# Kernel optimization log

Measured on AMD Instinct MI355X. Metric: run time of the kernel, lower is better.

## Reference

```python
import jax, jax.numpy as jnp
import numpy as np

C, L, M, DEPTH = 32, 4, 128, 7
DIM = (L ** (DEPTH + 1) - 1) // (L - 1)  # 21845 nodes, complete 4-ary tree, BFS order


def _level_starts(dim, fanout):
    # start offset of each BFS level of a complete `fanout`-ary tree
    starts = [0]
    n = 1
    while starts[-1] + n < dim:
        starts.append(starts[-1] + n)
        n *= fanout
    starts.append(dim)
    return starts  # level d occupies [starts[d], starts[d+1])


def setup_inputs() -> dict:
    key = jax.random.key(0)
    ks = jax.random.split(key, 5)
    return {
        "labels": jax.random.randint(ks[0], (DIM,), 0, M, dtype=jnp.int32),
        "A": jax.random.normal(ks[1], (C, C, L), jnp.float32),
        "B": jax.random.normal(ks[2], (C, M), jnp.float32),
        "Pi": jax.random.normal(ks[3], (C, L), jnp.float32),
        "SP": jax.random.normal(ks[4], (L,), jnp.float32),
    }


def _htmm_log_likelihood(labels, A, B, Pi, SP):
    dim = labels.shape[0]
    c, m = B.shape
    fan = A.shape[2]
    starts = _level_starts(dim, fan)
    D = len(starts) - 2  # deepest level index (leaves)

    # softmax reparameterization (dims as in torch source)
    smA = jax.nn.softmax(A, axis=0)   # (C,C,L)
    smB = jax.nn.softmax(B, axis=1)   # (C,M)
    smPi = jax.nn.softmax(Pi, axis=0)  # (C,L)
    smSP = jax.nn.softmax(SP, axis=0)  # (L,)

    n_leaves = starts[D + 1] - starts[D]
    leaf_pos = jnp.arange(n_leaves) % fan          # child position of each leaf
    leaf_labels = labels[starts[D]:]

    # ---- upward pass ----
    beta_leaf = smPi[:, leaf_pos].T * smB[:, leaf_labels].T  # (n_leaves,C)
    beta_leaf = beta_leaf / beta_leaf.sum(1, keepdims=True)
    beta = jnp.zeros((dim, c), A.dtype).at[starts[D]:].set(beta_leaf)
    t_beta = jnp.zeros((dim, c), A.dtype)
    A_SP = smA * smSP[None, None, :]  # (C,C,L): SP[pos] * A[:,:,pos]

    for d in range(D - 1, -1, -1):
        n_p = starts[d + 1] - starts[d]
        beta_ch = beta[starts[d + 1]:starts[d + 2]].reshape(n_p, fan, c)  # (P,L,C)
        # t_beta_u[i] = sum_l SP[l] * sum_j A[i,j,l] * beta_child_l[j]
        tb = jnp.einsum('ijl,plj->pi', A_SP, beta_ch)  # (P,C)
        bl = tb * smB[:, labels[starts[d]:starts[d + 1]]].T
        bl = bl / bl.sum(1, keepdims=True)
        t_beta = t_beta.at[starts[d]:starts[d + 1]].set(tb)
        beta = beta.at[starts[d]:starts[d + 1]].set(bl)

    # ---- downward pass ----
    eps = jnp.zeros((dim, c), A.dtype).at[0].set(beta[0])
    t_eps = jnp.zeros((dim, c, c, fan), A.dtype)
    for d in range(D):
        n_p = starts[d + 1] - starts[d]
        beta_ch = beta[starts[d + 1]:starts[d + 2]].reshape(n_p, fan, c)  # (P,L,C)
        eps_pa = eps[starts[d]:starts[d + 1]]    # (P,C)
        tb_pa = t_beta[starts[d]:starts[d + 1]]  # (P,C)
        # t_eps_u[j,i,l] = beta[ch_l,i] * SP[l]*A[j,i,l] * eps_u[j] / t_beta_u[j]
        te = (beta_ch.transpose(0, 2, 1)[:, None, :, :]   # (P,1,C_i,L)
              * A_SP[None]                                  # (1,C_j,C_i,L)
              * (eps_pa / tb_pa)[:, :, None, None])         # (P,C_j,1,1)
        t_eps = t_eps.at[starts[d]:starts[d + 1]].set(te)
        eps_ch = te.sum(1).transpose(0, 2, 1).reshape(-1, c)  # sum_j -> (P,L,C) -> (P*L,C)
        eps = eps.at[starts[d + 1]:starts[d + 2]].set(eps_ch)

    # ---- log-likelihood ----
    ll = (t_eps * jnp.log(smA)[None]).sum()
    ll = ll + (eps * jnp.log(smB)[:, labels].T).sum()
    ll = ll + (eps[starts[D]:] * jnp.log(smPi)[:, leaf_pos].T).sum()
    ll = ll + (t_eps * jnp.log(smSP)[None, None, None, :]).sum()
    return ll


def reference(labels, A, B, Pi, SP):
    return _htmm_log_likelihood(labels, A, B, Pi, SP)
```

## Files before the change

### kernel.cpp

```cpp
#include <hip/hip_runtime.h>


static constexpr int OFF_B4   = 0;
static constexpr int OFF_PART = 8192;
static constexpr int IC1      = 8704;
static constexpr int IROOT1   = 9216;
static constexpr int IREL     = 9248;
static constexpr int IC2      = 9760;
static constexpr int IROOT2   = 10272;

__device__ __forceinline__ float rsum32(float v) {
#pragma unroll
  for (int k = 1; k <= 16; k <<= 1) v += __shfl_xor(v, k);
  return v;
}
__device__ __forceinline__ void rsum32x2(float& a, float& b) {
#pragma unroll
  for (int k = 1; k <= 16; k <<= 1) { a += __shfl_xor(a, k); b += __shfl_xor(b, k); }
}
__device__ __forceinline__ void rsum32x4(float& a, float& b, float& c, float& d) {
#pragma unroll
  for (int k = 1; k <= 16; k <<= 1) {
    a += __shfl_xor(a, k); b += __shfl_xor(b, k);
    c += __shfl_xor(c, k); d += __shfl_xor(d, k);
  }
}
__device__ __forceinline__ float4 exp4f(float4 v) {
  return make_float4(__expf(v.x), __expf(v.y), __expf(v.z), __expf(v.w));
}

__device__ __forceinline__ float dot128(const float* Wr, const float* X) {
  float t0 = 0.f, t1 = 0.f, t2 = 0.f, t3 = 0.f;
#pragma unroll
  for (int j = 0; j < 32; ++j) {
    const float4 x = *(const float4*)(X + j * 4);
    t0 = fmaf(Wr[4 * j + 0], x.x, t0);
    t1 = fmaf(Wr[4 * j + 1], x.y, t1);
    t2 = fmaf(Wr[4 * j + 2], x.z, t2);
    t3 = fmaf(Wr[4 * j + 3], x.w, t3);
  }
  return (t0 + t1) + (t2 + t3);
}
__device__ __forceinline__ void dot128x2(const float* Wr, const float* X0,
                                         const float* X1, float& o0, float& o1) {
  float a0 = 0.f, a1 = 0.f, a2 = 0.f, a3 = 0.f;
  float b0 = 0.f, b1 = 0.f, b2 = 0.f, b3 = 0.f;
#pragma unroll
  for (int j = 0; j < 32; ++j) {
    const float4 x = *(const float4*)(X0 + j * 4);
    const float4 y = *(const float4*)(X1 + j * 4);
    a0 = fmaf(Wr[4 * j + 0], x.x, a0); b0 = fmaf(Wr[4 * j + 0], y.x, b0);
    a1 = fmaf(Wr[4 * j + 1], x.y, a1); b1 = fmaf(Wr[4 * j + 1], y.y, b1);
    a2 = fmaf(Wr[4 * j + 2], x.z, a2); b2 = fmaf(Wr[4 * j + 2], y.z, b2);
    a3 = fmaf(Wr[4 * j + 3], x.w, a3); b3 = fmaf(Wr[4 * j + 3], y.w, b3);
  }
  o0 = (a0 + a1) + (a2 + a3);
  o1 = (b0 + b1) + (b2 + b3);
}

__device__ __forceinline__ void wu128(const float* Wr, const float* ALG,
                                      const float* rb, int lane,
                                      float w[4], float u[4]) {
  w[0] = w[1] = w[2] = w[3] = 0.f;
  u[0] = u[1] = u[2] = u[3] = 0.f;
#pragma unroll
  for (int ii = 0; ii < 32; ii += 4) {
    const float4 rv = *(const float4*)(rb + ii);
#pragma unroll
    for (int di = 0; di < 4; ++di) {
      const int i = ii + di;
      const float rr = (di == 0) ? rv.x : (di == 1) ? rv.y : (di == 2) ? rv.z : rv.w;
      const float4 av = *(const float4*)(ALG + i * 128 + lane * 4);
      w[0] = fmaf(Wr[i * 4 + 0], rr, w[0]); u[0] = fmaf(av.x, rr, u[0]);
      w[1] = fmaf(Wr[i * 4 + 1], rr, w[1]); u[1] = fmaf(av.y, rr, u[1]);
      w[2] = fmaf(Wr[i * 4 + 2], rr, w[2]); u[2] = fmaf(av.z, rr, u[2]);
      w[3] = fmaf(Wr[i * 4 + 3], rr, w[3]); u[3] = fmaf(av.w, rr, u[3]);
    }
  }
}
__device__ __forceinline__ void wu128x2(const float* Wr, const float* ALG,
                                        const float* rb0, const float* rb1, int lane,
                                        float w0[4], float u0[4],
                                        float w1[4], float u1[4]) {
#pragma unroll
  for (int l = 0; l < 4; ++l) { w0[l] = u0[l] = w1[l] = u1[l] = 0.f; }
#pragma unroll
  for (int ii = 0; ii < 32; ii += 4) {
    const float4 r0 = *(const float4*)(rb0 + ii);
    const float4 r1 = *(const float4*)(rb1 + ii);
#pragma unroll
    for (int di = 0; di < 4; ++di) {
      const int i = ii + di;
      const float q0 = (di == 0) ? r0.x : (di == 1) ? r0.y : (di == 2) ? r0.z : r0.w;
      const float q1 = (di == 0) ? r1.x : (di == 1) ? r1.y : (di == 2) ? r1.z : r1.w;
      const float4 av = *(const float4*)(ALG + i * 128 + lane * 4);
      w0[0] = fmaf(Wr[i * 4 + 0], q0, w0[0]); w1[0] = fmaf(Wr[i * 4 + 0], q1, w1[0]);
      u0[0] = fmaf(av.x, q0, u0[0]);          u1[0] = fmaf(av.x, q1, u1[0]);
      w0[1] = fmaf(Wr[i * 4 + 1], q0, w0[1]); w1[1] = fmaf(Wr[i * 4 + 1], q1, w1[1]);
      u0[1] = fmaf(av.y, q0, u0[1]);          u1[1] = fmaf(av.y, q1, u1[1]);
      w0[2] = fmaf(Wr[i * 4 + 2], q0, w0[2]); w1[2] = fmaf(Wr[i * 4 + 2], q1, w1[2]);
      u0[2] = fmaf(av.z, q0, u0[2]);          u1[2] = fmaf(av.z, q1, u1[2]);
      w0[3] = fmaf(Wr[i * 4 + 3], q0, w0[3]); w1[3] = fmaf(Wr[i * 4 + 3], q1, w1[3]);
      u0[3] = fmaf(av.w, q0, u0[3]);          u1[3] = fmaf(av.w, q1, u1[3]);
    }
  }
}
__device__ __forceinline__ void wonly128(const float* Wr, const float* rb,
                                         float w[4]) {
  w[0] = w[1] = w[2] = w[3] = 0.f;
#pragma unroll
  for (int ii = 0; ii < 32; ii += 4) {
    const float4 rv = *(const float4*)(rb + ii);
#pragma unroll
    for (int di = 0; di < 4; ++di) {
      const int i = ii + di;
      const float rr = (di == 0) ? rv.x : (di == 1) ? rv.y : (di == 2) ? rv.z : rv.w;
      w[0] = fmaf(Wr[i * 4 + 0], rr, w[0]);
      w[1] = fmaf(Wr[i * 4 + 1], rr, w[1]);
      w[2] = fmaf(Wr[i * 4 + 2], rr, w[2]);
      w[3] = fmaf(Wr[i * 4 + 3], rr, w[3]);
    }
  }
}

__global__ __launch_bounds__(256, 1) void k_up(const int* __restrict__ labels,
                                               const float* __restrict__ A,
                                               const float* __restrict__ B,
                                               const float* __restrict__ Pi,
                                               const float* __restrict__ SP,
                                               float* __restrict__ ws) {
  __shared__ __align__(16) float scr[4224];
  __shared__ __align__(16) float regB[4224];
  __shared__ __align__(16) float sPt[132];
  __shared__ int labs[425];
  const int t = threadIdx.x, lane = t & 31, grp = t >> 5;
  const int s = blockIdx.x;
  const float4* A4 = (const float4*)A;
  const float4* B4 = (const float4*)B;

  const float sv0 = SP[0], sv1 = SP[1], sv2 = SP[2], sv3 = SP[3];
  const float sp0 = __expf(sv0), sp1 = __expf(sv1), sp2 = __expf(sv2), sp3 = __expf(sv3);
  const float spsum = sp0 + sp1 + sp2 + sp3;
  const float spinv = 1.f / spsum;
  float4 c4 = make_float4(0.f, 0.f, 0.f, 0.f);
  for (int i = 0; i < 32; ++i) {
    const float4 e = exp4f(A4[i * 32 + lane]);
    c4.x += e.x; c4.y += e.y; c4.z += e.z; c4.w += e.w;
  }
  const float4 inv4 = make_float4(sp0 * spinv / c4.x, sp1 * spinv / c4.y,
                                  sp2 * spinv / c4.z, sp3 * spinv / c4.w);
#pragma unroll
  for (int k = 0; k < 4; ++k) {
    const int i = grp * 4 + k;
    const float4 e = exp4f(A4[i * 32 + lane]);
    *(float4*)(scr + i * 132 + 4 * lane) =
        make_float4(e.x * inv4.x, e.y * inv4.y, e.z * inv4.z, e.w * inv4.w);
  }
#pragma unroll
  for (int rI = 0; rI < 4; ++rI) {
    const int i = grp + rI * 8;
    const float4 e = exp4f(B4[i * 32 + lane]);
    const float sinv = 1.f / rsum32(e.x + e.y + e.z + e.w);
    regB[(4 * lane + 0) * 33 + i] = e.x * sinv;
    regB[(4 * lane + 1) * 33 + i] = e.y * sinv;
    regB[(4 * lane + 2) * 33 + i] = e.z * sinv;
    regB[(4 * lane + 3) * 33 + i] = e.w * sinv;
  }
  if (grp < 4) {
    const float e = __expf(Pi[lane * 4 + grp]);
    sPt[grp * 33 + lane] = e / rsum32(e);
  }
  if (t < 84) {
    int g, d;
    if (t < 4) { g = 341 + 4 * s + t; d = 341 + t; }
    else if (t < 20) { g = 1365 + 16 * s + (t - 4); d = 345 + (t - 4); }
    else { g = 5461 + 64 * s + (t - 20); d = 361 + (t - 20); }
    labs[d] = labels[g];
  }
  if (t == 84) labs[85 + (s & 255)] = labels[85 + s];
  __syncthreads();
  float Wr[128];
#pragma unroll
  for (int j = 0; j < 32; ++j) {
    const float4 v = *(const float4*)(scr + lane * 132 + j * 4);
    Wr[4 * j] = v.x; Wr[4 * j + 1] = v.y; Wr[4 * j + 2] = v.z; Wr[4 * j + 3] = v.w;
  }
  __syncthreads();

#pragma unroll
  for (int h = 0; h < 2; ++h) {
    const int q0 = grp + 32 * h, q1 = q0 + 8, q2 = q0 + 16, q3 = q0 + 24;
    float v0 = sPt[(q0 & 3) * 33 + lane] * regB[labs[361 + q0] * 33 + lane];
    float v1 = sPt[(q1 & 3) * 33 + lane] * regB[labs[361 + q1] * 33 + lane];
    float v2 = sPt[(q2 & 3) * 33 + lane] * regB[labs[361 + q2] * 33 + lane];
    float v3 = sPt[(q3 & 3) * 33 + lane] * regB[labs[361 + q3] * 33 + lane];
    float s0 = v0, s1 = v1, s2 = v2, s3 = v3;
    rsum32x4(s0, s1, s2, s3);
    scr[(q0 >> 2) * 128 + lane * 4 + (q0 & 3)] = v0 / s0;
    scr[(q1 >> 2) * 128 + lane * 4 + (q1 & 3)] = v1 / s1;
    scr[(q2 >> 2) * 128 + lane * 4 + (q2 & 3)] = v2 / s2;
    scr[(q3 >> 2) * 128 + lane * 4 + (q3 & 3)] = v3 / s3;
  }
  __syncthreads();
  {
    const int p0 = grp, p1 = grp + 8;
    float tb0, tb1;
    dot128x2(Wr, scr + p0 * 128, scr + p1 * 128, tb0, tb1);
    float bl0 = tb0 * regB[labs[345 + p0] * 33 + lane];
    float bl1 = tb1 * regB[labs[345 + p1] * 33 + lane];
    float s0 = bl0, s1 = bl1;
    rsum32x2(s0, s1);
    bl0 /= s0; bl1 /= s1;
    scr[2048 + (p0 >> 2) * 128 + lane * 4 + (p0 & 3)] = bl0;
    scr[2048 + (p1 >> 2) * 128 + lane * 4 + (p1 & 3)] = bl1;
  }
  __syncthreads();
  if (grp < 4) {
    const float tb = dot128(Wr, scr + 2048 + grp * 128);
    float bl = tb * regB[labs[341 + grp] * 33 + lane];
    bl /= rsum32(bl);
    scr[2560 + lane * 4 + grp] = bl;
  }
  __syncthreads();
  if (grp == 0) {
    const float tb = dot128(Wr, scr + 2560);
    float bl = tb * regB[labs[85 + (s & 255)] * 33 + lane];
    bl /= rsum32(bl);
    ws[OFF_B4 + s * 32 + lane] = bl;
  }
}

__global__ __launch_bounds__(256, 1) void k_down(const int* __restrict__ labels,
                                                 const float* __restrict__ A,
                                                 const float* __restrict__ B,
                                                 const float* __restrict__ Pi,
                                                 const float* __restrict__ SP,
                                                 float* __restrict__ ws,
                                                 float* __restrict__ out) {
  __shared__ __align__(16) float scr[4224];
  __shared__ __align__(16) float regB[4224];
  __shared__ __align__(16) float sPt[132];
  __shared__ __align__(16) float tbrT[2720];
  __shared__ __align__(16) float tbS[672];
  __shared__ __align__(16) float ownb[32];
  __shared__ __align__(16) float r_buf[512];
  __shared__ int labs[425];
  __shared__ int fin;
  const int t = threadIdx.x, lane = t & 31, grp = t >> 5;
  const int s = blockIdx.x;
  int* wsi = (int*)ws;
  double* partd = (double*)(ws + OFF_PART);
  const float4* A4 = (const float4*)A;
  const float4* B4 = (const float4*)B;

  const float sv0 = SP[0], sv1 = SP[1], sv2 = SP[2], sv3 = SP[3];
  const float sp0 = __expf(sv0), sp1 = __expf(sv1), sp2 = __expf(sv2), sp3 = __expf(sv3);
  const float spsum = sp0 + sp1 + sp2 + sp3;
  const float spinv = 1.f / spsum;
  const float lss = __logf(spsum);
  float4 c4 = make_float4(0.f, 0.f, 0.f, 0.f);
  for (int i = 0; i < 32; ++i) {
    const float4 e = exp4f(A4[i * 32 + lane]);
    c4.x += e.x; c4.y += e.y; c4.z += e.z; c4.w += e.w;
  }
  const float4 inv4 = make_float4(sp0 * spinv / c4.x, sp1 * spinv / c4.y,
                                  sp2 * spinv / c4.z, sp3 * spinv / c4.w);
  const float4 sub4 = make_float4(__logf(c4.x) - (sv0 - lss), __logf(c4.y) - (sv1 - lss),
                                  __logf(c4.z) - (sv2 - lss), __logf(c4.w) - (sv3 - lss));
#pragma unroll
  for (int k = 0; k < 4; ++k) {
    const int i = grp * 4 + k;
    const float4 e = exp4f(A4[i * 32 + lane]);
    *(float4*)(scr + i * 132 + 4 * lane) =
        make_float4(e.x * inv4.x, e.y * inv4.y, e.z * inv4.z, e.w * inv4.w);
  }
#pragma unroll
  for (int rI = 0; rI < 4; ++rI) {
    const int i = grp + rI * 8;
    const float4 e = exp4f(B4[i * 32 + lane]);
    const float sinv = 1.f / rsum32(e.x + e.y + e.z + e.w);
    regB[(4 * lane + 0) * 33 + i] = e.x * sinv;
    regB[(4 * lane + 1) * 33 + i] = e.y * sinv;
    regB[(4 * lane + 2) * 33 + i] = e.z * sinv;
    regB[(4 * lane + 3) * 33 + i] = e.w * sinv;
  }
  if (grp < 4) {
    const float e = __expf(Pi[lane * 4 + grp]);
    sPt[grp * 33 + lane] = e / rsum32(e);
  }
  for (int idx = t; idx < 341; idx += 256) labs[idx] = labels[idx];
  if (t < 84) {
    int g, d;
    if (t < 4) { g = 341 + 4 * s + t; d = 341 + t; }
    else if (t < 20) { g = 1365 + 16 * s + (t - 4); d = 345 + (t - 4); }
    else { g = 5461 + 64 * s + (t - 20); d = 361 + (t - 20); }
    labs[d] = labels[g];
  }
  __syncthreads();
  float Wr[128];
#pragma unroll
  for (int j = 0; j < 32; ++j) {
    const float4 v = *(const float4*)(scr + lane * 132 + j * 4);
    Wr[4 * j] = v.x; Wr[4 * j + 1] = v.y; Wr[4 * j + 2] = v.z; Wr[4 * j + 3] = v.w;
  }
  __syncthreads();

#pragma unroll
  for (int h = 0; h < 2; ++h) {
    const int q0 = grp + 32 * h, q1 = q0 + 8, q2 = q0 + 16, q3 = q0 + 24;
    float v0 = sPt[(q0 & 3) * 33 + lane] * regB[labs[361 + q0] * 33 + lane];
    float v1 = sPt[(q1 & 3) * 33 + lane] * regB[labs[361 + q1] * 33 + lane];
    float v2 = sPt[(q2 & 3) * 33 + lane] * regB[labs[361 + q2] * 33 + lane];
    float v3 = sPt[(q3 & 3) * 33 + lane] * regB[labs[361 + q3] * 33 + lane];
    float s0 = v0, s1 = v1, s2 = v2, s3 = v3;
    rsum32x4(s0, s1, s2, s3);
    scr[(q0 >> 2) * 128 + lane * 4 + (q0 & 3)] = v0 / s0;
    scr[(q1 >> 2) * 128 + lane * 4 + (q1 & 3)] = v1 / s1;
    scr[(q2 >> 2) * 128 + lane * 4 + (q2 & 3)] = v2 / s2;
    scr[(q3 >> 2) * 128 + lane * 4 + (q3 & 3)] = v3 / s3;
  }
  __syncthreads();
  {
    const int p0 = grp, p1 = grp + 8;
    float tb0, tb1;
    dot128x2(Wr, scr + p0 * 128, scr + p1 * 128, tb0, tb1);
    float bl0 = tb0 * regB[labs[345 + p0] * 33 + lane];
    float bl1 = tb1 * regB[labs[345 + p1] * 33 + lane];
    float s0 = bl0, s1 = bl1;
    rsum32x2(s0, s1);
    bl0 /= s0; bl1 /= s1;
    tbS[(5 + p0) * 32 + lane] = tb0;
    tbS[(5 + p1) * 32 + lane] = tb1;
    scr[2048 + (p0 >> 2) * 128 + lane * 4 + (p0 & 3)] = bl0;
    scr[2048 + (p1 >> 2) * 128 + lane * 4 + (p1 & 3)] = bl1;
  }
  __syncthreads();
  if (grp < 4) {
    const float tb = dot128(Wr, scr + 2048 + grp * 128);
    float bl = tb * regB[labs[341 + grp] * 33 + lane];
    bl /= rsum32(bl);
    tbS[(1 + grp) * 32 + lane] = tb;
    scr[2560 + lane * 4 + grp] = bl;
  }
  __syncthreads();
  if (grp == 0) {
    const float tb = dot128(Wr, scr + 2560);
    float bl = tb * regB[labs[85 + s] * 33 + lane];
    bl /= rsum32(bl);
    tbS[lane] = tb;
    ownb[lane] = bl;
  }
  __syncthreads();

#pragma unroll
  for (int k = 0; k < 4; ++k) {
    const int p0 = grp + 16 * k, p1 = p0 + 8;
    float* st0 = scr + grp * 128;
    float* st1 = scr + 1024 + grp * 128;
#pragma unroll
    for (int l = 0; l < 4; ++l) {
      st0[lane * 4 + l] = ws[OFF_B4 + (p0 * 4 + l) * 32 + lane];
      st1[lane * 4 + l] = ws[OFF_B4 + (p1 * 4 + l) * 32 + lane];
    }
    float tb0, tb1;
    dot128x2(Wr, st0, st1, tb0, tb1);
    float bl0 = tb0 * regB[labs[21 + p0] * 33 + lane];
    float bl1 = tb1 * regB[labs[21 + p1] * 33 + lane];
    float s0 = bl0, s1 = bl1;
    rsum32x2(s0, s1);
    bl0 /= s0; bl1 /= s1;
    tbrT[(21 + p0) * 32 + lane] = tb0;
    tbrT[(21 + p1) * 32 + lane] = tb1;
    scr[2048 + (p0 >> 2) * 128 + lane * 4 + (p0 & 3)] = bl0;
    scr[2048 + (p1 >> 2) * 128 + lane * 4 + (p1 & 3)] = bl1;
  }
  __syncthreads();
  {
    const int p0 = grp, p1 = grp + 8;
    float tb0, tb1;
    dot128x2(Wr, scr + 2048 + p0 * 128, scr + 2048 + p1 * 128, tb0, tb1);
    float bl0 = tb0 * regB[labs[5 + p0] * 33 + lane];
    float bl1 = tb1 * regB[labs[5 + p1] * 33 + lane];
    float s0 = bl0, s1 = bl1;
    rsum32x2(s0, s1);
    bl0 /= s0; bl1 /= s1;
    tbrT[(5 + p0) * 32 + lane] = tb0;
    tbrT[(5 + p1) * 32 + lane] = tb1;
    scr[1024 + (p0 >> 2) * 128 + lane * 4 + (p0 & 3)] = bl0;
    scr[1024 + (p1 >> 2) * 128 + lane * 4 + (p1 & 3)] = bl1;
  }
  __syncthreads();
  if (grp < 4) {
    const float tb = dot128(Wr, scr + 1024 + grp * 128);
    float bl = tb * regB[labs[1 + grp] * 33 + lane];
    bl /= rsum32(bl);
    tbrT[(1 + grp) * 32 + lane] = tb;
    scr[1536 + lane * 4 + grp] = bl;
  }
  __syncthreads();
  if (grp == 0) tbrT[lane] = dot128(Wr, scr + 1536);
  __syncthreads();

  for (int idx = t; idx < 4224; idx += 256) regB[idx] = __logf(regB[idx]);
  if (t < 132) sPt[t] = __logf(sPt[t]);
#pragma unroll
  for (int i = 0; i < 32; ++i) {
    const float4 av = A4[i * 32 + lane];
    const float4 e = exp4f(av);
    const float4 asp = make_float4(e.x * inv4.x, e.y * inv4.y, e.z * inv4.z, e.w * inv4.w);
    Wr[i * 4 + 0] = asp.x; Wr[i * 4 + 1] = asp.y;
    Wr[i * 4 + 2] = asp.z; Wr[i * 4 + 3] = asp.w;
    if (grp == (i >> 2))
      *(float4*)(scr + i * 128 + lane * 4) =
          make_float4(asp.x * (av.x - sub4.x), asp.y * (av.y - sub4.y),
                      asp.z * (av.z - sub4.z), asp.w * (av.w - sub4.w));
  }
  __syncthreads();

  double ll = 0.0;
  float eps4own = 0.f;
  if (grp < 4) {
    const int n1 = 1 + (s >> 6), n2 = 5 + (s >> 4), n3 = 21 + (s >> 2);
    const int a0 = s >> 6, a1 = (s >> 4) & 3, a2 = (s >> 2) & 3, a3 = s & 3;
    float w[4], uv[4];
    float* rb = r_buf + grp * 32;

    float tbv = tbrT[lane];
    float bcv = tbv * __expf(regB[labs[0] * 33 + lane]);
    bcv /= rsum32(bcv);
    rb[lane] = bcv / tbv;
    if (grp == 0 && s == 0) {
      ll += (double)(bcv * regB[labs[0] * 33 + lane]);
      wu128(Wr, scr, rb, lane, w, uv);
      const float lb0 = regB[labs[1] * 33 + lane], lb1 = regB[labs[2] * 33 + lane];
      const float lb2 = regB[labs[3] * 33 + lane], lb3 = regB[labs[4] * 33 + lane];
      float b0 = tbrT[1 * 32 + lane] * __expf(lb0);
      float b1 = tbrT[2 * 32 + lane] * __expf(lb1);
      float b2 = tbrT[3 * 32 + lane] * __expf(lb2);
      float b3 = tbrT[4 * 32 + lane] * __expf(lb3);
      float s0 = b0, s1 = b1, s2 = b2, s3 = b3;
      rsum32x4(s0, s1, s2, s3);
      b0 /= s0; b1 /= s1; b2 /= s2; b3 /= s3;
      ll += (double)(b0 * uv[0]) + (double)(b0 * w[0] * lb0);
      ll += (double)(b1 * uv[1]) + (double)(b1 * w[1] * lb1);
      ll += (double)(b2 * uv[2]) + (double)(b2 * w[2] * lb2);
      ll += (double)(b3 * uv[3]) + (double)(b3 * w[3] * lb3);
    } else {
      wonly128(Wr, rb, w);
    }

    tbv = tbrT[n1 * 32 + lane];
    bcv = tbv * __expf(regB[labs[n1] * 33 + lane]);
    bcv /= rsum32(bcv);
    rb[lane] = (bcv * w[a0]) / tbv;
    if (grp == 1 && (s & 63) == 0) {
      wu128(Wr, scr, rb, lane, w, uv);
      const int cb = 5 + 4 * (s >> 6);
      const float lb0 = regB[labs[cb + 0] * 33 + lane], lb1 = regB[labs[cb + 1] * 33 + lane];
      const float lb2 = regB[labs[cb + 2] * 33 + lane], lb3 = regB[labs[cb + 3] * 33 + lane];
      float b0 = tbrT[(cb + 0) * 32 + lane] * __expf(lb0);
      float b1 = tbrT[(cb + 1) * 32 + lane] * __expf(lb1);
      float b2 = tbrT[(cb + 2) * 32 + lane] * __expf(lb2);
      float b3 = tbrT[(cb + 3) * 32 + lane] * __expf(lb3);
      float s0 = b0, s1 = b1, s2 = b2, s3 = b3;
      rsum32x4(s0, s1, s2, s3);
      b0 /= s0; b1 /= s1; b2 /= s2; b3 /= s3;
      ll += (double)(b0 * uv[0]) + (double)(b0 * w[0] * lb0);
      ll += (double)(b1 * uv[1]) + (double)(b1 * w[1] * lb1);
      ll += (double)(b2 * uv[2]) + (double)(b2 * w[2] * lb2);
      ll += (double)(b3 * uv[3]) + (double)(b3 * w[3] * lb3);
    } else {
      wonly128(Wr, rb, w);
    }

    tbv = tbrT[n2 * 32 + lane];
    bcv = tbv * __expf(regB[labs[n2] * 33 + lane]);
    bcv /= rsum32(bcv);
    rb[lane] = (bcv * w[a1]) / tbv;
    if (grp == 2 && (s & 15) == 0) {
      wu128(Wr, scr, rb, lane, w, uv);
      const int cb = 21 + 4 * (s >> 4);
      const float lb0 = regB[labs[cb + 0] * 33 + lane], lb1 = regB[labs[cb + 1] * 33 + lane];
      const float lb2 = regB[labs[cb + 2] * 33 + lane], lb3 = regB[labs[cb + 3] * 33 + lane];
      float b0 = tbrT[(cb + 0) * 32 + lane] * __expf(lb0);
      float b1 = tbrT[(cb + 1) * 32 + lane] * __expf(lb1);
      float b2 = tbrT[(cb + 2) * 32 + lane] * __expf(lb2);
      float b3 = tbrT[(cb + 3) * 32 + lane] * __expf(lb3);
      float s0 = b0, s1 = b1, s2 = b2, s3 = b3;
      rsum32x4(s0, s1, s2, s3);
      b0 /= s0; b1 /= s1; b2 /= s2; b3 /= s3;
      ll += (double)(b0 * uv[0]) + (double)(b0 * w[0] * lb0);
      ll += (double)(b1 * uv[1]) + (double)(b1 * w[1] * lb1);
      ll += (double)(b2 * uv[2]) + (double)(b2 * w[2] * lb2);
      ll += (double)(b3 * uv[3]) + (double)(b3 * w[3] * lb3);
    } else {
      wonly128(Wr, rb, w);
    }

    tbv = tbrT[n3 * 32 + lane];
    bcv = tbv * __expf(regB[labs[n3] * 33 + lane]);
    bcv /= rsum32(bcv);
    rb[lane] = (bcv * w[a2]) / tbv;
    if (grp == 3 && (s & 3) == 0) {
      wu128(Wr, scr, rb, lane, w, uv);
      const int cb = s & ~3;
#pragma unroll
      for (int l = 0; l < 4; ++l) {
        const int ci = cb + l;
        const float bc = ws[OFF_B4 + ci * 32 + lane];
        const float e = bc * w[l];
        ll += (double)(bc * uv[l]) + (double)(e * regB[labs[85 + ci] * 33 + lane]);
      }
    } else {
      wonly128(Wr, rb, w);
    }
    eps4own = ownb[lane] * w[a3];
  }
  __syncthreads();

  if (grp == 0) {
    r_buf[lane] = eps4own / tbS[lane];
    float w[4], u[4];
    wu128(Wr, scr, r_buf, lane, w, u);
#pragma unroll
    for (int l = 0; l < 4; ++l) {
      const int lab = labs[341 + l];
      const float tbv = tbS[(1 + l) * 32 + lane];
      float bcv = tbv * __expf(regB[lab * 33 + lane]);
      bcv /= rsum32(bcv);
      const float e = bcv * w[l];
      ll += (double)(bcv * u[l]) + (double)(e * regB[lab * 33 + lane]);
      tbS[(1 + l) * 32 + lane] = e / tbv;
    }
  }
  __syncthreads();
  if (grp < 4) {
    const int p = grp;
    r_buf[p * 32 + lane] = tbS[(1 + p) * 32 + lane];
    float w[4], u[4];
    wu128(Wr, scr, r_buf + p * 32, lane, w, u);
#pragma unroll
    for (int l = 0; l < 4; ++l) {
      const int q = p * 4 + l;
      const int lab = labs[345 + q];
      const float tbv = tbS[(5 + q) * 32 + lane];
      float bcv = tbv * __expf(regB[lab * 33 + lane]);
      bcv /= rsum32(bcv);
      const float e = bcv * w[l];
      ll += (double)(bcv * u[l]) + (double)(e * regB[lab * 33 + lane]);
      tbS[(5 + q) * 32 + lane] = e / tbv;
    }
  }
  __syncthreads();
  {
    const int p0 = grp, p1 = grp + 8;
    float* rb0 = r_buf + grp * 32;
    float* rb1 = r_buf + 256 + grp * 32;
    rb0[lane] = tbS[(5 + p0) * 32 + lane];
    rb1[lane] = tbS[(5 + p1) * 32 + lane];
    float w0[4], u0[4], w1[4], u1[4];
    wu128x2(Wr, scr, rb0, rb1, lane, w0, u0, w1, u1);
#pragma unroll
    for (int l = 0; l < 4; ++l) {
      const int q0 = p0 * 4 + l, q1 = p1 * 4 + l;
      const float lb0 = regB[labs[361 + q0] * 33 + lane];
      const float lb1 = regB[labs[361 + q1] * 33 + lane];
      const float lp = sPt[l * 33 + lane];
      float b0 = __expf(lp + lb0);
      float b1 = __expf(lp + lb1);
      float s0 = b0, s1 = b1;
      rsum32x2(s0, s1);
      b0 /= s0; b1 /= s1;
      const float e0 = b0 * w0[l], e1 = b1 * w1[l];
      ll += (double)(b0 * u0[l]) + (double)(e0 * lb0) + (double)(e0 * lp);
      ll += (double)(b1 * u1[l]) + (double)(e1 * lb1) + (double)(e1 * lp);
    }
  }

#pragma unroll
  for (int k = 32; k >= 1; k >>= 1) ll += __shfl_xor(ll, k);
  double* rbd = (double*)r_buf;
  __syncthreads();
  if ((t & 63) == 0) rbd[t >> 6] = ll;
  __syncthreads();
  if (t == 0) {
    partd[s] = (rbd[0] + rbd[1]) + (rbd[2] + rbd[3]);
    __threadfence();
    int f = 0;
    if (atomicAdd(&wsi[IC2 + 32 * (s >> 4)], 1) == 15)
      if (atomicAdd(&wsi[IROOT2], 1) == 15) f = 1;
    fin = f;
  }
  __syncthreads();
  if (fin) {
    __threadfence();
    if (t < 64) {
      double v = 0.0;
      for (int k = t; k < 256; k += 64) v += partd[k];
#pragma unroll
      for (int k = 32; k >= 1; k >>= 1) v += __shfl_xor(v, k);
      if (t == 0) out[0] = (float)v;
    }
  }
}

extern "C" void kernel_launch(void* const* d_in, const int* in_sizes, int n_in,
                              void* d_out, int out_size, void* d_ws, size_t ws_size,
                              hipStream_t stream) {
  (void)in_sizes; (void)n_in; (void)out_size; (void)ws_size;
  const int* labels = (const int*)d_in[0];
  const float* A = (const float*)d_in[1];
  const float* B = (const float*)d_in[2];
  const float* Pi = (const float*)d_in[3];
  const float* SP = (const float*)d_in[4];
  float* ws = (float*)d_ws;
  float* out = (float*)d_out;

  hipMemsetAsync((char*)d_ws + IC1 * 4, 0, (IROOT2 + 1 - IC1) * 4, stream);
  hipLaunchKernelGGL(k_up, dim3(256), dim3(256), 0, stream,
                     labels, A, B, Pi, SP, ws);
  hipLaunchKernelGGL(k_down, dim3(256), dim3(256), 0, stream,
                     labels, A, B, Pi, SP, ws, out);
}
```

Measured before the change: 116.6 us.

## Double k_down block to 512 threads and zero counters in-kernel instead of memset

The down-pass kernel now runs 512 threads (16 groups) per block, spreading the per-block work for level recomputation, A/B softmax setup and the leaf loops over twice as many wavefronts. The scratch layout grows to hold the wider staging. The host memset of the completion counters is removed; k_up zeroes them at its start, dropping one launch from the stream. The risks are higher register pressure from the 128-float Wr array at 512 threads per block, and some regions still use only 8 of the 16 groups.

```diff
diff --git a/kernel.cpp b/kernel.cpp
--- a/kernel.cpp
+++ b/kernel.cpp
@@ -3,9 +3,6 @@
 
 static constexpr int OFF_B4   = 0;
 static constexpr int OFF_PART = 8192;
-static constexpr int IC1      = 8704;
-static constexpr int IROOT1   = 9216;
-static constexpr int IREL     = 9248;
 static constexpr int IC2      = 9760;
 static constexpr int IROOT2   = 10272;
 
@@ -135,8 +132,12 @@
   __shared__ int labs[425];
   const int t = threadIdx.x, lane = t & 31, grp = t >> 5;
   const int s = blockIdx.x;
+  int* wsi = (int*)ws;
   const float4* A4 = (const float4*)A;
   const float4* B4 = (const float4*)B;
+
+  if (t < 16) wsi[IC2 + 32 * t] = 0;
+  else if (t == 16) wsi[IROOT2] = 0;
 
   const float sv0 = SP[0], sv1 = SP[1], sv2 = SP[2], sv3 = SP[3];
   const float sp0 = __expf(sv0), sp1 = __expf(sv1), sp2 = __expf(sv2), sp3 = __expf(sv3);
@@ -230,14 +231,14 @@
   }
 }
 
-__global__ __launch_bounds__(256, 1) void k_down(const int* __restrict__ labels,
+__global__ __launch_bounds__(512, 1) void k_down(const int* __restrict__ labels,
                                                  const float* __restrict__ A,
                                                  const float* __restrict__ B,
                                                  const float* __restrict__ Pi,
                                                  const float* __restrict__ SP,
                                                  float* __restrict__ ws,
                                                  float* __restrict__ out) {
-  __shared__ __align__(16) float scr[4224];
+  __shared__ __align__(16) float scr[6144];
   __shared__ __align__(16) float regB[4224];
   __shared__ __align__(16) float sPt[132];
   __shared__ __align__(16) float tbrT[2720];
@@ -268,15 +269,15 @@
   const float4 sub4 = make_float4(__logf(c4.x) - (sv0 - lss), __logf(c4.y) - (sv1 - lss),
                                   __logf(c4.z) - (sv2 - lss), __logf(c4.w) - (sv3 - lss));
 #pragma unroll
-  for (int k = 0; k < 4; ++k) {
-    const int i = grp * 4 + k;
+  for (int k = 0; k < 2; ++k) {
+    const int i = grp * 2 + k;
     const float4 e = exp4f(A4[i * 32 + lane]);
     *(float4*)(scr + i * 132 + 4 * lane) =
         make_float4(e.x * inv4.x, e.y * inv4.y, e.z * inv4.z, e.w * inv4.w);
   }
 #pragma unroll
-  for (int rI = 0; rI < 4; ++rI) {
-    const int i = grp + rI * 8;
+  for (int rI = 0; rI < 2; ++rI) {
+    const int i = grp + rI * 16;
     const float4 e = exp4f(B4[i * 32 + lane]);
     const float sinv = 1.f / rsum32(e.x + e.y + e.z + e.w);
     regB[(4 * lane + 0) * 33 + i] = e.x * sinv;
@@ -288,7 +289,7 @@
     const float e = __expf(Pi[lane * 4 + grp]);
     sPt[grp * 33 + lane] = e / rsum32(e);
   }
-  for (int idx = t; idx < 341; idx += 256) labs[idx] = labels[idx];
+  for (int idx = t; idx < 341; idx += 512) labs[idx] = labels[idx];
   if (t < 84) {
     int g, d;
     if (t < 4) { g = 341 + 4 * s + t; d = 341 + t; }
@@ -305,9 +306,8 @@
   }
   __syncthreads();
 
-#pragma unroll
-  for (int h = 0; h < 2; ++h) {
-    const int q0 = grp + 32 * h, q1 = q0 + 8, q2 = q0 + 16, q3 = q0 + 24;
+  {
+    const int q0 = grp, q1 = grp + 16, q2 = grp + 32, q3 = grp + 48;
     float v0 = sPt[(q0 & 3) * 33 + lane] * regB[labs[361 + q0] * 33 + lane];
     float v1 = sPt[(q1 & 3) * 33 + lane] * regB[labs[361 + q1] * 33 + lane];
     float v2 = sPt[(q2 & 3) * 33 + lane] * regB[labs[361 + q2] * 33 + lane];
@@ -320,7 +320,7 @@
     scr[(q3 >> 2) * 128 + lane * 4 + (q3 & 3)] = v3 / s3;
   }
   __syncthreads();
-  {
+  if (grp < 8) {
     const int p0 = grp, p1 = grp + 8;
     float tb0, tb1;
     dot128x2(Wr, scr + p0 * 128, scr + p1 * 128, tb0, tb1);
@@ -353,10 +353,10 @@
   __syncthreads();
 
 #pragma unroll
-  for (int k = 0; k < 4; ++k) {
-    const int p0 = grp + 16 * k, p1 = p0 + 8;
+  for (int h = 0; h < 2; ++h) {
+    const int p0 = grp + 32 * h, p1 = p0 + 16;
     float* st0 = scr + grp * 128;
-    float* st1 = scr + 1024 + grp * 128;
+    float* st1 = scr + 2048 + grp * 128;
 #pragma unroll
     for (int l = 0; l < 4; ++l) {
       st0[lane * 4 + l] = ws[OFF_B4 + (p0 * 4 + l) * 32 + lane];
@@ -371,37 +371,31 @@
     bl0 /= s0; bl1 /= s1;
     tbrT[(21 + p0) * 32 + lane] = tb0;
     tbrT[(21 + p1) * 32 + lane] = tb1;
-    scr[2048 + (p0 >> 2) * 128 + lane * 4 + (p0 & 3)] = bl0;
-    scr[2048 + (p1 >> 2) * 128 + lane * 4 + (p1 & 3)] = bl1;
+    scr[4096 + (p0 >> 2) * 128 + lane * 4 + (p0 & 3)] = bl0;
+    scr[4096 + (p1 >> 2) * 128 + lane * 4 + (p1 & 3)] = bl1;
   }
   __syncthreads();
   {
-    const int p0 = grp, p1 = grp + 8;
-    float tb0, tb1;
-    dot128x2(Wr, scr + 2048 + p0 * 128, scr + 2048 + p1 * 128, tb0, tb1);
-    float bl0 = tb0 * regB[labs[5 + p0] * 33 + lane];
-    float bl1 = tb1 * regB[labs[5 + p1] * 33 + lane];
-    float s0 = bl0, s1 = bl1;
-    rsum32x2(s0, s1);
-    bl0 /= s0; bl1 /= s1;
-    tbrT[(5 + p0) * 32 + lane] = tb0;
-    tbrT[(5 + p1) * 32 + lane] = tb1;
-    scr[1024 + (p0 >> 2) * 128 + lane * 4 + (p0 & 3)] = bl0;
-    scr[1024 + (p1 >> 2) * 128 + lane * 4 + (p1 & 3)] = bl1;
+    const int p = grp;
+    const float tb = dot128(Wr, scr + 4096 + p * 128);
+    float bl = tb * regB[labs[5 + p] * 33 + lane];
+    bl /= rsum32(bl);
+    tbrT[(5 + p) * 32 + lane] = tb;
+    scr[(p >> 2) * 128 + lane * 4 + (p & 3)] = bl;
   }
   __syncthreads();
   if (grp < 4) {
-    const float tb = dot128(Wr, scr + 1024 + grp * 128);
+    const float tb = dot128(Wr, scr + grp * 128);
     float bl = tb * regB[labs[1 + grp] * 33 + lane];
     bl /= rsum32(bl);
     tbrT[(1 + grp) * 32 + lane] = tb;
-    scr[1536 + lane * 4 + grp] = bl;
-  }
-  __syncthreads();
-  if (grp == 0) tbrT[lane] = dot128(Wr, scr + 1536);
-  __syncthreads();
-
-  for (int idx = t; idx < 4224; idx += 256) regB[idx] = __logf(regB[idx]);
+    scr[512 + lane * 4 + grp] = bl;
+  }
+  __syncthreads();
+  if (grp == 0) tbrT[lane] = dot128(Wr, scr + 512);
+  __syncthreads();
+
+  for (int idx = t; idx < 4224; idx += 512) regB[idx] = __logf(regB[idx]);
   if (t < 132) sPt[t] = __logf(sPt[t]);
 #pragma unroll
   for (int i = 0; i < 32; ++i) {
@@ -410,7 +404,7 @@
     const float4 asp = make_float4(e.x * inv4.x, e.y * inv4.y, e.z * inv4.z, e.w * inv4.w);
     Wr[i * 4 + 0] = asp.x; Wr[i * 4 + 1] = asp.y;
     Wr[i * 4 + 2] = asp.z; Wr[i * 4 + 3] = asp.w;
-    if (grp == (i >> 2))
+    if (grp == (i >> 1))
       *(float4*)(scr + i * 128 + lane * 4) =
           make_float4(asp.x * (av.x - sub4.x), asp.y * (av.y - sub4.y),
                       asp.z * (av.z - sub4.z), asp.w * (av.w - sub4.w));
@@ -552,7 +546,7 @@
     }
   }
   __syncthreads();
-  {
+  if (grp < 8) {
     const int p0 = grp, p1 = grp + 8;
     float* rb0 = r_buf + grp * 32;
     float* rb1 = r_buf + 256 + grp * 32;
@@ -584,7 +578,8 @@
   if ((t & 63) == 0) rbd[t >> 6] = ll;
   __syncthreads();
   if (t == 0) {
-    partd[s] = (rbd[0] + rbd[1]) + (rbd[2] + rbd[3]);
+    partd[s] = ((rbd[0] + rbd[1]) + (rbd[2] + rbd[3])) +
+               ((rbd[4] + rbd[5]) + (rbd[6] + rbd[7]));
     __threadfence();
     int f = 0;
     if (atomicAdd(&wsi[IC2 + 32 * (s >> 4)], 1) == 15)
@@ -616,9 +611,8 @@
   float* ws = (float*)d_ws;
   float* out = (float*)d_out;
 
-  hipMemsetAsync((char*)d_ws + IC1 * 4, 0, (IROOT2 + 1 - IC1) * 4, stream);
   hipLaunchKernelGGL(k_up, dim3(256), dim3(256), 0, stream,
                      labels, A, B, Pi, SP, ws);
-  hipLaunchKernelGGL(k_down, dim3(256), dim3(256), 0, stream,
+  hipLaunchKernelGGL(k_down, dim3(256), dim3(512), 0, stream,
                      labels, A, B, Pi, SP, ws, out);
 }
```

After: 109.5 us. 1.06x faster.
